# Optimization experiments

Hardware: AMD Instinct MI355X
Metric: run time of the kernel (lower is better)

The kernel has to match this reference:

```python
import jax, jax.numpy as jnp
import numpy as np

H = 128
NUM_GRAPHS = 256
NUM_TASKS = 40
BN_EPS = 1e-5


def setup_inputs() -> dict:
    key = jax.random.key(0)
    ks = jax.random.split(key, 32)
    N, E, F = 50000, 600000, 9
    inp = {}
    inp["x"] = jax.random.randint(ks[0], (N, 1), 0, 2)
    inp["edge_index"] = jax.random.randint(ks[1], (2, E), 0, N)
    inp["edge_attr"] = jax.random.uniform(ks[2], (E, F), dtype=jnp.float32)
    inp["batch"] = jnp.sort(jax.random.randint(ks[3], (N,), 0, NUM_GRAPHS))
    inp["self_loop_index"] = 7
    inp["self_loop_type"] = 1
    # parameters
    s = 0.02
    inp["node_emb"] = jax.random.normal(ks[4], (2, H), jnp.float32) * s
    for l in range(2):
        o = 5 + l * 11
        inp[f"enc_w{l}"] = jax.random.normal(ks[o + 0], (F, H), jnp.float32) * s
        inp[f"enc_b{l}"] = jnp.zeros((H,), jnp.float32)
        inp[f"w1_{l}"] = jax.random.normal(ks[o + 1], (2 * H, 2 * H), jnp.float32) * s
        inp[f"b1_{l}"] = jnp.zeros((2 * H,), jnp.float32)
        inp[f"gamma{l}"] = jnp.ones((2 * H,), jnp.float32)
        inp[f"beta{l}"] = jnp.zeros((2 * H,), jnp.float32)
        inp[f"mean{l}"] = jax.random.normal(ks[o + 2], (2 * H,), jnp.float32) * 0.1
        inp[f"var{l}"] = jax.random.uniform(ks[o + 3], (2 * H,), jnp.float32, 0.5, 1.5)
        inp[f"w2_{l}"] = jax.random.normal(ks[o + 4], (2 * H, H), jnp.float32) * s
        inp[f"b2_{l}"] = jnp.zeros((H,), jnp.float32)
    inp["pred_w"] = jax.random.normal(ks[30], (2 * H, NUM_TASKS), jnp.float32) * s
    inp["pred_b"] = jnp.zeros((NUM_TASKS,), jnp.float32)
    return inp


def _gin_layer(h, ei, ea, N, enc_w, enc_b, w1, b1, gamma, beta, mean, var, w2, b2):
    # edge encode: Linear(F, H) on all (real + self-loop) edges
    e = ea @ enc_w + enc_b                                  # [E+N, H]
    msg = jnp.concatenate([h[ei[1]], e], axis=1)            # [E+N, 2H] (feature_concat)
    agg = jax.ops.segment_sum(msg, ei[0], num_segments=N)   # sum pooling -> [N, 2H]
    z = agg @ w1 + b1
    z = (z - mean) * jax.lax.rsqrt(var + BN_EPS) * gamma + beta  # BatchNorm1d (eval)
    z = jax.nn.relu(z)
    return z @ w2 + b2                                      # [N, H]


def reference(x, edge_index, edge_attr, batch, self_loop_index, self_loop_type,
              node_emb,
              enc_w0, enc_b0, w1_0, b1_0, gamma0, beta0, mean0, var0, w2_0, b2_0,
              enc_w1, enc_b1, w1_1, b1_1, gamma1, beta1, mean1, var1, w2_1, b2_1,
              pred_w, pred_b):
    N = x.shape[0]
    loop = jnp.arange(N, dtype=edge_index.dtype)
    ei = jnp.concatenate([edge_index, jnp.stack([loop, loop])], axis=1)  # add self loops
    sl_attr = jnp.zeros((N, edge_attr.shape[1]), edge_attr.dtype).at[:, self_loop_index].set(
        jnp.asarray(self_loop_type, edge_attr.dtype))
    ea = jnp.concatenate([edge_attr, sl_attr], axis=0)       # [E+N, F]

    h0 = node_emb[x.reshape(-1)]                             # input node embedding [N, H]
    h1 = jax.nn.relu(_gin_layer(h0, ei, ea, N, enc_w0, enc_b0, w1_0, b1_0,
                                gamma0, beta0, mean0, var0, w2_0, b2_0))
    h2 = _gin_layer(h1, ei, ea, N, enc_w1, enc_b1, w1_1, b1_1,
                    gamma1, beta1, mean1, var1, w2_1, b2_1)  # JK='last'

    # graph mean pooling over batch ids
    sums = jax.ops.segment_sum(h2, batch, num_segments=NUM_GRAPHS)
    cnt = jax.ops.segment_sum(jnp.ones((N,), h2.dtype), batch, num_segments=NUM_GRAPHS)
    pooled = sums / jnp.maximum(cnt, 1.0)[:, None]
    graph_rep = jnp.concatenate([pooled, pooled], axis=1)    # no center_node_idx
    return graph_rep @ pred_w + pred_b                       # [G, num_tasks]
```

## Files before the change

kernel.cpp:

```cpp
#include <hip/hip_runtime.h>

#define H   128
#define H2  256
#define NG  256
#define NT  40
#define NF  9

typedef __attribute__((ext_vector_type(8))) short short8;
typedef __attribute__((ext_vector_type(4))) float f32x4;

#define MFMA16(a, b, c) __builtin_amdgcn_mfma_f32_16x16x32_bf16(a, b, c, 0, 0, 0)

__device__ __forceinline__ void f2bf_hilo(float x, unsigned short& hi, unsigned short& lo) {
  unsigned u = __float_as_uint(x);
  unsigned hh = (u + 0x7FFFu + ((u >> 16) & 1u)) >> 16;
  float hf = __uint_as_float(hh << 16);
  float r = x - hf;
  unsigned v = __float_as_uint(r);
  unsigned ll = (v + 0x7FFFu + ((v >> 16) & 1u)) >> 16;
  hi = (unsigned short)hh;
  lo = (unsigned short)ll;
}

__device__ __forceinline__ void cvt8(float4 a, float4 b, short8& hi, short8& lo) {
  float xs[8] = {a.x, a.y, a.z, a.w, b.x, b.y, b.z, b.w};
#pragma unroll
  for (int j = 0; j < 8; j++) {
    unsigned short h, l;
    f2bf_hilo(xs[j], h, l);
    hi[j] = (short)h;
    lo[j] = (short)l;
  }
}

__global__ void k_degc(const int* __restrict__ ei, const int* __restrict__ x,
                       unsigned* __restrict__ degc, int E) {
  int e = blockIdx.x * blockDim.x + threadIdx.x;
  if (e >= E) return;
  int dst = ei[e], src = ei[E + e];
  atomicAdd(&degc[dst], 1u + ((unsigned)x[src] << 16));
}

__global__ __launch_bounds__(1024) void k_scan(const unsigned* __restrict__ degc,
                                               unsigned* __restrict__ off,
                                               unsigned* __restrict__ cur, int N) {
  __shared__ unsigned wsum[16];
  __shared__ unsigned wpre[16];
  __shared__ unsigned s_run;
  int tid = threadIdx.x;
  int lane = tid & 63, wv = tid >> 6;
  if (tid == 0) s_run = 0u;
  __syncthreads();
  for (int base = 0; base < N; base += 4096) {
    int i0 = base + tid * 4;
    unsigned v0 = 0, v1 = 0, v2 = 0, v3 = 0;
    if (i0 + 0 < N) v0 = degc[i0 + 0] & 0xFFFFu;
    if (i0 + 1 < N) v1 = degc[i0 + 1] & 0xFFFFu;
    if (i0 + 2 < N) v2 = degc[i0 + 2] & 0xFFFFu;
    if (i0 + 3 < N) v3 = degc[i0 + 3] & 0xFFFFu;
    unsigned tsum = v0 + v1 + v2 + v3;
    unsigned sc = tsum;
#pragma unroll
    for (int d = 1; d < 64; d <<= 1) {
      unsigned t = __shfl_up(sc, d);
      if (lane >= d) sc += t;
    }
    if (lane == 63) wsum[wv] = sc;
    __syncthreads();
    if (wv == 0 && lane < 16) {
      unsigned xv = wsum[lane];
#pragma unroll
      for (int d = 1; d < 16; d <<= 1) {
        unsigned t = __shfl_up(xv, d);
        if (lane >= d) xv += t;
      }
      wpre[lane] = xv;
    }
    __syncthreads();
    unsigned excl = s_run + (wv ? wpre[wv - 1] : 0u) + (sc - tsum);
    unsigned p1 = excl + v0, p2 = p1 + v1, p3 = p2 + v2;
    if (i0 + 0 < N) { off[i0 + 0] = excl; cur[i0 + 0] = excl; }
    if (i0 + 1 < N) { off[i0 + 1] = p1;   cur[i0 + 1] = p1; }
    if (i0 + 2 < N) { off[i0 + 2] = p2;   cur[i0 + 2] = p2; }
    if (i0 + 3 < N) { off[i0 + 3] = p3;   cur[i0 + 3] = p3; }
    __syncthreads();
    if (tid == 0) s_run += wpre[15];
  }
  if (tid == 0) off[N] = s_run;
}

__global__ void k_scatter(const int* __restrict__ ei, unsigned* __restrict__ cur,
                          int* __restrict__ csrc, int* __restrict__ ceid, int E) {
  int e = blockIdx.x * blockDim.x + threadIdx.x;
  if (e >= E) return;
  int dst = ei[e], src = ei[E + e];
  unsigned pos = atomicAdd(&cur[dst], 1u);
  csrc[pos] = src;
  ceid[pos] = e;
}

__global__ __launch_bounds__(256) void k_S(const float* __restrict__ ea,
    const unsigned* __restrict__ off, const int* __restrict__ ceid,
    float* __restrict__ S, int N) {
  int lane = threadIdx.x & 63;
  int wv = threadIdx.x >> 6;
  int sub = lane & 7;
  int v = blockIdx.x * 32 + wv * 8 + (lane >> 3);
  if (v >= N) return;
  unsigned o = off[v], e = off[v + 1];
  float acc[NF];
#pragma unroll
  for (int f = 0; f < NF; f++) acc[f] = 0.f;
  for (unsigned i = o + sub; i < e; i += 8) {
    const float* a = ea + (size_t)ceid[i] * NF;
#pragma unroll
    for (int f = 0; f < NF; f++) acc[f] += a[f];
  }
#pragma unroll
  for (int d = 1; d < 8; d <<= 1)
#pragma unroll
    for (int f = 0; f < NF; f++) acc[f] += __shfl_xor(acc[f], d);
  if (sub == 0) {
#pragma unroll
    for (int f = 0; f < NF; f++) S[(size_t)v * NF + f] = acc[f];
  }
}

__global__ __launch_bounds__(256) void k_gather(const float* __restrict__ h,
    const unsigned* __restrict__ off, const int* __restrict__ csrc,
    float* __restrict__ hs, int N) {
  int v = blockIdx.x * 4 + (threadIdx.x >> 6);
  int lane = threadIdx.x & 63;
  if (v >= N) return;
  unsigned o = off[v], e = off[v + 1];
  const float2* hp = (const float2*)h;
  float2 acc = hp[(size_t)v * 64 + lane];
  float2 a0 = {0.f, 0.f}, a1 = {0.f, 0.f}, a2 = {0.f, 0.f}, a3 = {0.f, 0.f};
  unsigned i = o;
  for (; i + 4 <= e; i += 4) {
    int s0 = csrc[i], s1 = csrc[i + 1], s2 = csrc[i + 2], s3 = csrc[i + 3];
    float2 t0 = hp[(size_t)s0 * 64 + lane];
    float2 t1 = hp[(size_t)s1 * 64 + lane];
    float2 t2 = hp[(size_t)s2 * 64 + lane];
    float2 t3 = hp[(size_t)s3 * 64 + lane];
    a0.x += t0.x; a0.y += t0.y;
    a1.x += t1.x; a1.y += t1.y;
    a2.x += t2.x; a2.y += t2.y;
    a3.x += t3.x; a3.y += t3.y;
  }
  for (; i < e; i++) {
    float2 t = hp[(size_t)csrc[i] * 64 + lane];
    acc.x += t.x; acc.y += t.y;
  }
  acc.x += (a0.x + a1.x) + (a2.x + a3.x);
  acc.y += (a0.y + a1.y) + (a2.y + a3.y);
  ((float2*)hs)[(size_t)v * 64 + lane] = acc;
}

__global__ void k_prepA0(const float* __restrict__ emb,
                         const float* __restrict__ enc_w, const float* __restrict__ enc_b,
                         const float* __restrict__ w1, const float* __restrict__ b1,
                         const float* __restrict__ gamma, const float* __restrict__ beta,
                         const float* __restrict__ mean, const float* __restrict__ var,
                         const int* __restrict__ sli, const int* __restrict__ slt,
                         unsigned short* __restrict__ BAhi, unsigned short* __restrict__ BAlo,
                         float* __restrict__ cc) {
  int c = threadIdx.x;
  float e0 = 0.f, e1 = 0.f, u = 0.f;
  float m[NF];
#pragma unroll
  for (int f = 0; f < NF; f++) m[f] = 0.f;
  for (int k = 0; k < H; k++) {
    float wt = w1[(size_t)k * H2 + c];
    e0 += emb[k] * wt;
    e1 += emb[H + k] * wt;
    float wb = w1[(size_t)(H + k) * H2 + c];
#pragma unroll
    for (int f = 0; f < NF; f++) m[f] += enc_w[f * H + k] * wb;
    u += enc_b[k] * wb;
  }
  float k0 = (float)(*slt) * m[*sli] + u + b1[c];
  float scv = gamma[c] * rsqrtf(var[c] + 1e-5f);
  cc[c] = scv;
  cc[H2 + c] = beta[c] - mean[c] * scv;
  int ct = c >> 4, cl = c & 15;
  for (int k = 0; k < 32; k++) {
    float val;
    if (k == 0)       val = e0;
    else if (k == 1)  val = e1;
    else if (k < 11)  val = m[k - 2];
    else if (k == 11) val = u;
    else if (k == 12) val = k0;
    else              val = 0.f;
    unsigned short h, l;
    f2bf_hilo(val, h, l);
    int lane = (k >> 3) * 16 + cl, j = k & 7;
    size_t idx = ((size_t)(ct * 64 + lane)) * 8 + j;
    BAhi[idx] = h;
    BAlo[idx] = l;
  }
}

__global__ void k_prepA1(const float* __restrict__ enc_w, const float* __restrict__ enc_b,
                         const float* __restrict__ w1, const float* __restrict__ b1,
                         const float* __restrict__ gamma, const float* __restrict__ beta,
                         const float* __restrict__ mean, const float* __restrict__ var,
                         const int* __restrict__ sli, const int* __restrict__ slt,
                         unsigned short* __restrict__ BAhi, unsigned short* __restrict__ BAlo,
                         float* __restrict__ cc) {
  int c = threadIdx.x;
  float m[NF];
  float u = 0.f;
#pragma unroll
  for (int f = 0; f < NF; f++) m[f] = 0.f;
  for (int k = 0; k < H; k++) {
    float wv = w1[(size_t)(H + k) * H2 + c];
#pragma unroll
    for (int f = 0; f < NF; f++) m[f] += enc_w[f * H + k] * wv;
    u += enc_b[k] * wv;
  }
  float k0 = (float)(*slt) * m[*sli] + u + b1[c];
  float scv = gamma[c] * rsqrtf(var[c] + 1e-5f);
  cc[c] = scv;
  cc[H2 + c] = beta[c] - mean[c] * scv;
  int ct = c >> 4, cl = c & 15;
  for (int k = 0; k < 160; k++) {
    float val;
    if (k < 128)      val = w1[(size_t)k * H2 + c];
    else if (k < 137) val = m[k - 128];
    else if (k == 137) val = u;
    else if (k == 138) val = k0;
    else              val = 0.f;
    unsigned short h, l;
    f2bf_hilo(val, h, l);
    int ks = k >> 5, kr = k & 31;
    int lane = (kr >> 3) * 16 + cl, j = kr & 7;
    size_t idx = ((size_t)((ks * 16 + ct) * 64 + lane)) * 8 + j;
    BAhi[idx] = h;
    BAlo[idx] = l;
  }
}

__global__ void k_prepB2(const float* __restrict__ w2,
                         unsigned short* __restrict__ BBhi, unsigned short* __restrict__ BBlo) {
  int t = threadIdx.x;
  int c = t & 127, half = t >> 7;
  int ct = c >> 4, cl = c & 15;
  for (int kk = 0; kk < 128; kk++) {
    int k = half * 128 + kk;
    float val = w2[(size_t)k * H + c];
    unsigned short h, l;
    f2bf_hilo(val, h, l);
    int ks = k >> 5, kr = k & 31;
    int lane = (kr >> 3) * 16 + cl, j = kr & 7;
    size_t idx = ((size_t)((ks * 8 + ct) * 64 + lane)) * 8 + j;
    BBhi[idx] = h;
    BBlo[idx] = l;
  }
}

__global__ __launch_bounds__(256) void k_layer(
    const float* __restrict__ hs, const float* __restrict__ S,
    const unsigned* __restrict__ degc, const int* __restrict__ x,
    const unsigned short* __restrict__ BAhi, const unsigned short* __restrict__ BAlo,
    const unsigned short* __restrict__ BBhi, const unsigned short* __restrict__ BBlo,
    const float* __restrict__ cc, const float* __restrict__ b2,
    float* __restrict__ out, const int* __restrict__ batch,
    int N, int relu_out, int pool, int nks) {
  __shared__ float ext[32][36];
  __shared__ unsigned short zhi[32 * 256];
  __shared__ unsigned short zlo[32 * 256];
  int tid = threadIdx.x;
  int row0 = blockIdx.x * 32;

  for (int i = tid; i < 32 * 36; i += 256) {
    int r = i / 36, c2 = i - r * 36;
    int v = row0 + r;
    float val = 0.f;
    if (v < N) {
      unsigned pk = degc[v];
      float dg = (float)(pk & 0xFFFFu);
      float c1 = (float)(pk >> 16);
      if (nks == 0) {
        if (c2 == 0)       val = (dg - c1) + ((x[v] == 0) ? 1.f : 0.f);
        else if (c2 == 1)  val = c1 + ((x[v] != 0) ? 1.f : 0.f);
        else if (c2 < 11)  val = S[(size_t)v * NF + (c2 - 2)];
        else if (c2 == 11) val = dg;
        else if (c2 == 12) val = 1.0f;
      } else {
        if (c2 < NF)       val = S[(size_t)v * NF + c2];
        else if (c2 == 9)  val = dg;
        else if (c2 == 10) val = 1.0f;
      }
    }
    ext[r][c2] = val;
  }
  __syncthreads();

  int l = tid & 63, wv = tid >> 6;
  int rowoff = (wv >> 1) * 16;
  int ctoffA = (wv & 1) * 8;
  int lr = l & 15, lg = l >> 4;

  f32x4 acc[8];
#pragma unroll
  for (int ct = 0; ct < 8; ct++) acc[ct] = f32x4{0.f, 0.f, 0.f, 0.f};

  if (nks) {
#pragma unroll
    for (int ks = 0; ks < 4; ks++) {
      int row = row0 + rowoff + lr;
      int rowc = row < N ? row : N - 1;
      const float* src = hs + (size_t)rowc * H + ks * 32 + lg * 8;
      float4 x0 = ((const float4*)src)[0];
      float4 x1 = ((const float4*)src)[1];
      short8 ahi, alo;
      cvt8(x0, x1, ahi, alo);
#pragma unroll
      for (int ct = 0; ct < 8; ct++) {
        int gct = ctoffA + ct;
        short8 bhi = ((const short8*)BAhi)[((ks * 16 + gct) << 6) + l];
        short8 blo = ((const short8*)BAlo)[((ks * 16 + gct) << 6) + l];
        acc[ct] = MFMA16(ahi, bhi, acc[ct]);
        acc[ct] = MFMA16(ahi, blo, acc[ct]);
        acc[ct] = MFMA16(alo, bhi, acc[ct]);
      }
    }
  }
  {
    const float* src = &ext[rowoff + lr][lg * 8];
    float4 x0 = ((const float4*)src)[0];
    float4 x1 = ((const float4*)src)[1];
    short8 ahi, alo;
    cvt8(x0, x1, ahi, alo);
#pragma unroll
    for (int ct = 0; ct < 8; ct++) {
      int gct = ctoffA + ct;
      short8 bhi = ((const short8*)BAhi)[((nks * 16 + gct) << 6) + l];
      short8 blo = ((const short8*)BAlo)[((nks * 16 + gct) << 6) + l];
      acc[ct] = MFMA16(ahi, bhi, acc[ct]);
      acc[ct] = MFMA16(ahi, blo, acc[ct]);
      acc[ct] = MFMA16(alo, bhi, acc[ct]);
    }
  }

#pragma unroll
  for (int ct = 0; ct < 8; ct++) {
    int c = (ctoffA + ct) * 16 + lr;
    float scv = cc[c], shv = cc[H2 + c];
#pragma unroll
    for (int r = 0; r < 4; r++) {
      float z = acc[ct][r] * scv + shv;
      z = fmaxf(z, 0.f);
      unsigned short h, lo2;
      f2bf_hilo(z, h, lo2);
      int zr = rowoff + lg * 4 + r;
      unsigned off = (unsigned)(zr * 512 + c * 2) ^ (unsigned)((zr & 7) << 4);
      *(unsigned short*)((char*)zhi + off) = h;
      *(unsigned short*)((char*)zlo + off) = lo2;
    }
  }
  __syncthreads();

  f32x4 acc2[4];
#pragma unroll
  for (int ct = 0; ct < 4; ct++) acc2[ct] = f32x4{0.f, 0.f, 0.f, 0.f};
#pragma unroll
  for (int ks = 0; ks < 8; ks++) {
    int zr = rowoff + lr;
    unsigned off = (unsigned)(zr * 512 + (ks * 32 + lg * 8) * 2) ^ (unsigned)((zr & 7) << 4);
    short8 ahi = *(const short8*)((char*)zhi + off);
    short8 alo = *(const short8*)((char*)zlo + off);
#pragma unroll
    for (int ct = 0; ct < 4; ct++) {
      int gct = (wv & 1) * 4 + ct;
      short8 bhi = ((const short8*)BBhi)[((ks * 8 + gct) << 6) + l];
      short8 blo = ((const short8*)BBlo)[((ks * 8 + gct) << 6) + l];
      acc2[ct] = MFMA16(ahi, bhi, acc2[ct]);
      acc2[ct] = MFMA16(ahi, blo, acc2[ct]);
      acc2[ct] = MFMA16(alo, bhi, acc2[ct]);
    }
  }

#pragma unroll
  for (int ct = 0; ct < 4; ct++) {
    int c2 = ((wv & 1) * 4 + ct) * 16 + lr;
    float bias = b2[c2];
#pragma unroll
    for (int r = 0; r < 4; r++) {
      int row = row0 + rowoff + lg * 4 + r;
      if (row >= N) continue;
      float val = acc2[ct][r] + bias;
      if (relu_out) val = fmaxf(val, 0.f);
      if (pool) {
        atomicAdd(&out[(size_t)batch[row] * H + c2], val);
      } else {
        out[(size_t)row * H + c2] = val;
      }
    }
  }
}

__global__ void k_cnt(const int* __restrict__ batch, float* __restrict__ cnt, int N) {
  int v = blockIdx.x * blockDim.x + threadIdx.x;
  if (v < N) atomicAdd(&cnt[batch[v]], 1.0f);
}

__global__ void k_pred(const float* __restrict__ pooled, const float* __restrict__ cnt,
                       const float* __restrict__ pw, const float* __restrict__ pb,
                       float* __restrict__ outp) {
  int g = blockIdx.x;
  int t = threadIdx.x;
  if (t >= NT) return;
  float acc = 0.f;
  for (int k = 0; k < H; k++)
    acc += pooled[(size_t)g * H + k] * (pw[k * NT + t] + pw[(H + k) * NT + t]);
  float c = fmaxf(cnt[g], 1.0f);
  outp[(size_t)g * NT + t] = acc / c + pb[t];
}

extern "C" void kernel_launch(void* const* d_in, const int* in_sizes, int n_in,
                              void* d_out, int out_size, void* d_ws, size_t ws_size,
                              hipStream_t stream) {
  const int*   x     = (const int*)d_in[0];
  const int*   ei    = (const int*)d_in[1];
  const float* ea    = (const float*)d_in[2];
  const int*   batch = (const int*)d_in[3];
  const int*   sli   = (const int*)d_in[4];
  const int*   slt   = (const int*)d_in[5];
  const float* emb   = (const float*)d_in[6];
  const float* encw[2] = {(const float*)d_in[7],  (const float*)d_in[17]};
  const float* encb[2] = {(const float*)d_in[8],  (const float*)d_in[18]};
  const float* w1[2]   = {(const float*)d_in[9],  (const float*)d_in[19]};
  const float* b1[2]   = {(const float*)d_in[10], (const float*)d_in[20]};
  const float* gam[2]  = {(const float*)d_in[11], (const float*)d_in[21]};
  const float* bet[2]  = {(const float*)d_in[12], (const float*)d_in[22]};
  const float* mea[2]  = {(const float*)d_in[13], (const float*)d_in[23]};
  const float* var[2]  = {(const float*)d_in[14], (const float*)d_in[24]};
  const float* w2[2]   = {(const float*)d_in[15], (const float*)d_in[25]};
  const float* b2[2]   = {(const float*)d_in[16], (const float*)d_in[26]};
  const float* pw = (const float*)d_in[27];
  const float* pb = (const float*)d_in[28];

  int N = in_sizes[0];
  int E = in_sizes[1] / 2;

  char* p = (char*)d_ws;
  auto alloc = [&](size_t bytes) {
    char* r = p;
    p += (bytes + 255) / 256 * 256;
    return r;
  };
  unsigned* degc   = (unsigned*)alloc((size_t)N * 4);
  float*    S      = (float*)alloc((size_t)N * NF * 4);
  unsigned* off    = (unsigned*)alloc((size_t)(N + 1) * 4);
  unsigned* cur    = (unsigned*)alloc((size_t)N * 4);
  int*      csrc   = (int*)alloc((size_t)E * 4);
  int*      ceid   = (int*)alloc((size_t)E * 4);
  float*    hB     = (float*)alloc((size_t)N * H * 4);
  float*    hS     = (float*)alloc((size_t)N * H * 4);
  unsigned short* BA0hi = (unsigned short*)alloc((size_t)16 * 64 * 8 * 2);
  unsigned short* BA0lo = (unsigned short*)alloc((size_t)16 * 64 * 8 * 2);
  unsigned short* BA1hi = (unsigned short*)alloc((size_t)5 * 16 * 64 * 8 * 2);
  unsigned short* BA1lo = (unsigned short*)alloc((size_t)5 * 16 * 64 * 8 * 2);
  unsigned short* BB0hi = (unsigned short*)alloc((size_t)8 * 8 * 64 * 8 * 2);
  unsigned short* BB0lo = (unsigned short*)alloc((size_t)8 * 8 * 64 * 8 * 2);
  unsigned short* BB1hi = (unsigned short*)alloc((size_t)8 * 8 * 64 * 8 * 2);
  unsigned short* BB1lo = (unsigned short*)alloc((size_t)8 * 8 * 64 * 8 * 2);
  float*    cc0    = (float*)alloc((size_t)2 * H2 * 4);
  float*    cc1    = (float*)alloc((size_t)2 * H2 * 4);
  float*    pooled = (float*)alloc((size_t)NG * H * 4);
  float*    cnt    = (float*)alloc((size_t)NG * 4);

  hipMemsetAsync(degc, 0, (size_t)N * 4, stream);
  hipMemsetAsync(pooled, 0, (size_t)NG * H * 4, stream);
  hipMemsetAsync(cnt, 0, (size_t)NG * 4, stream);

  int nblk = (N + 31) / 32;

  k_degc<<<(E + 255) / 256, 256, 0, stream>>>(ei, x, degc, E);
  k_scan<<<1, 1024, 0, stream>>>(degc, off, cur, N);
  k_scatter<<<(E + 255) / 256, 256, 0, stream>>>(ei, cur, csrc, ceid, E);
  k_S<<<(N + 31) / 32, 256, 0, stream>>>(ea, off, ceid, S, N);

  k_prepA0<<<1, 256, 0, stream>>>(emb, encw[0], encb[0], w1[0], b1[0], gam[0], bet[0],
                                  mea[0], var[0], sli, slt, BA0hi, BA0lo, cc0);
  k_prepB2<<<1, 256, 0, stream>>>(w2[0], BB0hi, BB0lo);
  k_prepA1<<<1, 256, 0, stream>>>(encw[1], encb[1], w1[1], b1[1], gam[1], bet[1],
                                  mea[1], var[1], sli, slt, BA1hi, BA1lo, cc1);
  k_prepB2<<<1, 256, 0, stream>>>(w2[1], BB1hi, BB1lo);

  k_layer<<<nblk, 256, 0, stream>>>(nullptr, S, degc, x, BA0hi, BA0lo, BB0hi, BB0lo,
                                    cc0, b2[0], hB, batch, N, 1, 0, 0);
  k_gather<<<(N + 3) / 4, 256, 0, stream>>>(hB, off, csrc, hS, N);
  k_layer<<<nblk, 256, 0, stream>>>(hS, S, degc, x, BA1hi, BA1lo, BB1hi, BB1lo,
                                    cc1, b2[1], pooled, batch, N, 0, 1, 4);

  k_cnt<<<(N + 255) / 256, 256, 0, stream>>>(batch, cnt, N);
  k_pred<<<NG, 64, 0, stream>>>(pooled, cnt, pw, pb, (float*)d_out);
}
```

Measured before the change: 679.9 us.

## Retile layer GEMM to 64 rows, emit bf16 hi/lo from gather, vectorize loads

The fused layer kernel now handles 64 rows per block. Each wave reuses its B fragments across four row fragments in the first GEMM and across two in the second, which cuts repeated global weight loads. The gather kernel unrolls to eight independent neighbor loads and writes its sums as split bf16 hi/lo arrays, so the layer kernel reads ready-made MFMA operands instead of converting fp32. The edge-attribute sum loads use wider vector reads. In exchange, shared memory per block doubles, the grid has fewer blocks, and register pressure rises, which can lower occupancy.

```diff
diff --git a/kernel.cpp b/kernel.cpp
--- a/kernel.cpp
+++ b/kernel.cpp
@@ -8,6 +8,8 @@
 
 typedef __attribute__((ext_vector_type(8))) short short8;
 typedef __attribute__((ext_vector_type(4))) float f32x4;
+typedef float float4u __attribute__((ext_vector_type(4)));
+typedef float4u float4ua __attribute__((aligned(4)));
 
 #define MFMA16(a, b, c) __builtin_amdgcn_mfma_f32_16x16x32_bf16(a, b, c, 0, 0, 0)
 
@@ -113,8 +115,12 @@
   for (int f = 0; f < NF; f++) acc[f] = 0.f;
   for (unsigned i = o + sub; i < e; i += 8) {
     const float* a = ea + (size_t)ceid[i] * NF;
-#pragma unroll
-    for (int f = 0; f < NF; f++) acc[f] += a[f];
+    float4u v0 = ((const float4ua*)a)[0];
+    float4u v1 = ((const float4ua*)a)[1];
+    float v8 = a[8];
+    acc[0] += v0.x; acc[1] += v0.y; acc[2] += v0.z; acc[3] += v0.w;
+    acc[4] += v1.x; acc[5] += v1.y; acc[6] += v1.z; acc[7] += v1.w;
+    acc[8] += v8;
   }
 #pragma unroll
   for (int d = 1; d < 8; d <<= 1)
@@ -128,33 +134,38 @@
 
 __global__ __launch_bounds__(256) void k_gather(const float* __restrict__ h,
     const unsigned* __restrict__ off, const int* __restrict__ csrc,
-    float* __restrict__ hs, int N) {
+    unsigned short* __restrict__ hsHi, unsigned short* __restrict__ hsLo, int N) {
   int v = blockIdx.x * 4 + (threadIdx.x >> 6);
   int lane = threadIdx.x & 63;
   if (v >= N) return;
   unsigned o = off[v], e = off[v + 1];
   const float2* hp = (const float2*)h;
   float2 acc = hp[(size_t)v * 64 + lane];
-  float2 a0 = {0.f, 0.f}, a1 = {0.f, 0.f}, a2 = {0.f, 0.f}, a3 = {0.f, 0.f};
+  float2 a[8];
+#pragma unroll
+  for (int j = 0; j < 8; j++) a[j] = make_float2(0.f, 0.f);
   unsigned i = o;
-  for (; i + 4 <= e; i += 4) {
-    int s0 = csrc[i], s1 = csrc[i + 1], s2 = csrc[i + 2], s3 = csrc[i + 3];
-    float2 t0 = hp[(size_t)s0 * 64 + lane];
-    float2 t1 = hp[(size_t)s1 * 64 + lane];
-    float2 t2 = hp[(size_t)s2 * 64 + lane];
-    float2 t3 = hp[(size_t)s3 * 64 + lane];
-    a0.x += t0.x; a0.y += t0.y;
-    a1.x += t1.x; a1.y += t1.y;
-    a2.x += t2.x; a2.y += t2.y;
-    a3.x += t3.x; a3.y += t3.y;
+  for (; i + 8 <= e; i += 8) {
+    int s[8];
+#pragma unroll
+    for (int j = 0; j < 8; j++) s[j] = csrc[i + j];
+#pragma unroll
+    for (int j = 0; j < 8; j++) {
+      float2 t = hp[(size_t)s[j] * 64 + lane];
+      a[j].x += t.x; a[j].y += t.y;
+    }
   }
   for (; i < e; i++) {
     float2 t = hp[(size_t)csrc[i] * 64 + lane];
     acc.x += t.x; acc.y += t.y;
   }
-  acc.x += (a0.x + a1.x) + (a2.x + a3.x);
-  acc.y += (a0.y + a1.y) + (a2.y + a3.y);
-  ((float2*)hs)[(size_t)v * 64 + lane] = acc;
+#pragma unroll
+  for (int j = 0; j < 8; j++) { acc.x += a[j].x; acc.y += a[j].y; }
+  unsigned short h0, l0, h1, l1;
+  f2bf_hilo(acc.x, h0, l0);
+  f2bf_hilo(acc.y, h1, l1);
+  ((unsigned*)hsHi)[(size_t)v * 64 + lane] = (unsigned)h0 | ((unsigned)h1 << 16);
+  ((unsigned*)hsLo)[(size_t)v * 64 + lane] = (unsigned)l0 | ((unsigned)l1 << 16);
 }
 
 __global__ void k_prepA0(const float* __restrict__ emb,
@@ -260,21 +271,22 @@
 }
 
 __global__ __launch_bounds__(256) void k_layer(
-    const float* __restrict__ hs, const float* __restrict__ S,
-    const unsigned* __restrict__ degc, const int* __restrict__ x,
+    const unsigned short* __restrict__ hsHi, const unsigned short* __restrict__ hsLo,
+    const float* __restrict__ S, const unsigned* __restrict__ degc,
+    const int* __restrict__ x,
     const unsigned short* __restrict__ BAhi, const unsigned short* __restrict__ BAlo,
     const unsigned short* __restrict__ BBhi, const unsigned short* __restrict__ BBlo,
     const float* __restrict__ cc, const float* __restrict__ b2,
     float* __restrict__ out, const int* __restrict__ batch,
     int N, int relu_out, int pool, int nks) {
-  __shared__ float ext[32][36];
-  __shared__ unsigned short zhi[32 * 256];
-  __shared__ unsigned short zlo[32 * 256];
+  __shared__ float ext[64][36];
+  __shared__ unsigned short zhi[64 * 256];
+  __shared__ unsigned short zlo[64 * 256];
   int tid = threadIdx.x;
-  int row0 = blockIdx.x * 32;
-
-  for (int i = tid; i < 32 * 36; i += 256) {
-    int r = i / 36, c2 = i - r * 36;
+  int row0 = blockIdx.x * 64;
+
+  for (int i = tid; i < 64 * 32; i += 256) {
+    int r = i >> 5, c2 = i & 31;
     int v = row0 + r;
     float val = 0.f;
     if (v < N) {
@@ -298,104 +310,141 @@
   __syncthreads();
 
   int l = tid & 63, wv = tid >> 6;
-  int rowoff = (wv >> 1) * 16;
-  int ctoffA = (wv & 1) * 8;
   int lr = l & 15, lg = l >> 4;
 
-  f32x4 acc[8];
-#pragma unroll
-  for (int ct = 0; ct < 8; ct++) acc[ct] = f32x4{0.f, 0.f, 0.f, 0.f};
+  f32x4 acc[4][4];
+#pragma unroll
+  for (int rf = 0; rf < 4; rf++)
+#pragma unroll
+    for (int ct = 0; ct < 4; ct++) acc[rf][ct] = f32x4{0.f, 0.f, 0.f, 0.f};
 
   if (nks) {
 #pragma unroll
     for (int ks = 0; ks < 4; ks++) {
-      int row = row0 + rowoff + lr;
-      int rowc = row < N ? row : N - 1;
-      const float* src = hs + (size_t)rowc * H + ks * 32 + lg * 8;
+      short8 ah[4], al[4];
+#pragma unroll
+      for (int rf = 0; rf < 4; rf++) {
+        int row = row0 + rf * 16 + lr;
+        int rowc = row < N ? row : N - 1;
+        ah[rf] = *(const short8*)(hsHi + (size_t)rowc * H + ks * 32 + lg * 8);
+        al[rf] = *(const short8*)(hsLo + (size_t)rowc * H + ks * 32 + lg * 8);
+      }
+      short8 bh[4], bl[4];
+#pragma unroll
+      for (int ct = 0; ct < 4; ct++) {
+        int gct = wv * 4 + ct;
+        bh[ct] = ((const short8*)BAhi)[((ks * 16 + gct) << 6) + l];
+        bl[ct] = ((const short8*)BAlo)[((ks * 16 + gct) << 6) + l];
+      }
+#pragma unroll
+      for (int ct = 0; ct < 4; ct++)
+#pragma unroll
+        for (int rf = 0; rf < 4; rf++) {
+          acc[rf][ct] = MFMA16(ah[rf], bh[ct], acc[rf][ct]);
+          acc[rf][ct] = MFMA16(ah[rf], bl[ct], acc[rf][ct]);
+          acc[rf][ct] = MFMA16(al[rf], bh[ct], acc[rf][ct]);
+        }
+    }
+  }
+  {
+    short8 ah[4], al[4];
+#pragma unroll
+    for (int rf = 0; rf < 4; rf++) {
+      const float* src = &ext[rf * 16 + lr][lg * 8];
       float4 x0 = ((const float4*)src)[0];
       float4 x1 = ((const float4*)src)[1];
-      short8 ahi, alo;
-      cvt8(x0, x1, ahi, alo);
-#pragma unroll
-      for (int ct = 0; ct < 8; ct++) {
-        int gct = ctoffA + ct;
-        short8 bhi = ((const short8*)BAhi)[((ks * 16 + gct) << 6) + l];
-        short8 blo = ((const short8*)BAlo)[((ks * 16 + gct) << 6) + l];
-        acc[ct] = MFMA16(ahi, bhi, acc[ct]);
-        acc[ct] = MFMA16(ahi, blo, acc[ct]);
-        acc[ct] = MFMA16(alo, bhi, acc[ct]);
-      }
-    }
-  }
-  {
-    const float* src = &ext[rowoff + lr][lg * 8];
-    float4 x0 = ((const float4*)src)[0];
-    float4 x1 = ((const float4*)src)[1];
-    short8 ahi, alo;
-    cvt8(x0, x1, ahi, alo);
-#pragma unroll
-    for (int ct = 0; ct < 8; ct++) {
-      int gct = ctoffA + ct;
-      short8 bhi = ((const short8*)BAhi)[((nks * 16 + gct) << 6) + l];
-      short8 blo = ((const short8*)BAlo)[((nks * 16 + gct) << 6) + l];
-      acc[ct] = MFMA16(ahi, bhi, acc[ct]);
-      acc[ct] = MFMA16(ahi, blo, acc[ct]);
-      acc[ct] = MFMA16(alo, bhi, acc[ct]);
-    }
-  }
-
-#pragma unroll
-  for (int ct = 0; ct < 8; ct++) {
-    int c = (ctoffA + ct) * 16 + lr;
+      cvt8(x0, x1, ah[rf], al[rf]);
+    }
+    short8 bh[4], bl[4];
+#pragma unroll
+    for (int ct = 0; ct < 4; ct++) {
+      int gct = wv * 4 + ct;
+      bh[ct] = ((const short8*)BAhi)[((nks * 16 + gct) << 6) + l];
+      bl[ct] = ((const short8*)BAlo)[((nks * 16 + gct) << 6) + l];
+    }
+#pragma unroll
+    for (int ct = 0; ct < 4; ct++)
+#pragma unroll
+      for (int rf = 0; rf < 4; rf++) {
+        acc[rf][ct] = MFMA16(ah[rf], bh[ct], acc[rf][ct]);
+        acc[rf][ct] = MFMA16(ah[rf], bl[ct], acc[rf][ct]);
+        acc[rf][ct] = MFMA16(al[rf], bh[ct], acc[rf][ct]);
+      }
+  }
+
+#pragma unroll
+  for (int ct = 0; ct < 4; ct++) {
+    int c = (wv * 4 + ct) * 16 + lr;
     float scv = cc[c], shv = cc[H2 + c];
 #pragma unroll
-    for (int r = 0; r < 4; r++) {
-      float z = acc[ct][r] * scv + shv;
-      z = fmaxf(z, 0.f);
-      unsigned short h, lo2;
-      f2bf_hilo(z, h, lo2);
-      int zr = rowoff + lg * 4 + r;
-      unsigned off = (unsigned)(zr * 512 + c * 2) ^ (unsigned)((zr & 7) << 4);
-      *(unsigned short*)((char*)zhi + off) = h;
-      *(unsigned short*)((char*)zlo + off) = lo2;
+    for (int rf = 0; rf < 4; rf++) {
+#pragma unroll
+      for (int r = 0; r < 4; r++) {
+        float z = acc[rf][ct][r] * scv + shv;
+        z = fmaxf(z, 0.f);
+        unsigned short h, lo2;
+        f2bf_hilo(z, h, lo2);
+        int zr = rf * 16 + lg * 4 + r;
+        unsigned off = (unsigned)(zr * 512 + c * 2) ^ (unsigned)((zr & 7) << 4);
+        *(unsigned short*)((char*)zhi + off) = h;
+        *(unsigned short*)((char*)zlo + off) = lo2;
+      }
     }
   }
   __syncthreads();
 
-  f32x4 acc2[4];
-#pragma unroll
-  for (int ct = 0; ct < 4; ct++) acc2[ct] = f32x4{0.f, 0.f, 0.f, 0.f};
+  int r0b = (wv >> 1) * 32;
+  int cb = wv & 1;
+  f32x4 acc2[2][4];
+#pragma unroll
+  for (int rf = 0; rf < 2; rf++)
+#pragma unroll
+    for (int ct = 0; ct < 4; ct++) acc2[rf][ct] = f32x4{0.f, 0.f, 0.f, 0.f};
+
 #pragma unroll
   for (int ks = 0; ks < 8; ks++) {
-    int zr = rowoff + lr;
-    unsigned off = (unsigned)(zr * 512 + (ks * 32 + lg * 8) * 2) ^ (unsigned)((zr & 7) << 4);
-    short8 ahi = *(const short8*)((char*)zhi + off);
-    short8 alo = *(const short8*)((char*)zlo + off);
+    short8 zah[2], zal[2];
+#pragma unroll
+    for (int rf = 0; rf < 2; rf++) {
+      int zr = r0b + rf * 16 + lr;
+      unsigned off = (unsigned)(zr * 512 + (ks * 32 + lg * 8) * 2) ^ (unsigned)((zr & 7) << 4);
+      zah[rf] = *(const short8*)((char*)zhi + off);
+      zal[rf] = *(const short8*)((char*)zlo + off);
+    }
+    short8 bh[4], bl[4];
 #pragma unroll
     for (int ct = 0; ct < 4; ct++) {
-      int gct = (wv & 1) * 4 + ct;
-      short8 bhi = ((const short8*)BBhi)[((ks * 8 + gct) << 6) + l];
-      short8 blo = ((const short8*)BBlo)[((ks * 8 + gct) << 6) + l];
-      acc2[ct] = MFMA16(ahi, bhi, acc2[ct]);
-      acc2[ct] = MFMA16(ahi, blo, acc2[ct]);
-      acc2[ct] = MFMA16(alo, bhi, acc2[ct]);
-    }
+      int gct = cb * 4 + ct;
+      bh[ct] = ((const short8*)BBhi)[((ks * 8 + gct) << 6) + l];
+      bl[ct] = ((const short8*)BBlo)[((ks * 8 + gct) << 6) + l];
+    }
+#pragma unroll
+    for (int ct = 0; ct < 4; ct++)
+#pragma unroll
+      for (int rf = 0; rf < 2; rf++) {
+        acc2[rf][ct] = MFMA16(zah[rf], bh[ct], acc2[rf][ct]);
+        acc2[rf][ct] = MFMA16(zah[rf], bl[ct], acc2[rf][ct]);
+        acc2[rf][ct] = MFMA16(zal[rf], bh[ct], acc2[rf][ct]);
+      }
   }
 
 #pragma unroll
   for (int ct = 0; ct < 4; ct++) {
-    int c2 = ((wv & 1) * 4 + ct) * 16 + lr;
+    int c2 = (cb * 4 + ct) * 16 + lr;
     float bias = b2[c2];
 #pragma unroll
-    for (int r = 0; r < 4; r++) {
-      int row = row0 + rowoff + lg * 4 + r;
-      if (row >= N) continue;
-      float val = acc2[ct][r] + bias;
-      if (relu_out) val = fmaxf(val, 0.f);
-      if (pool) {
-        atomicAdd(&out[(size_t)batch[row] * H + c2], val);
-      } else {
-        out[(size_t)row * H + c2] = val;
+    for (int rf = 0; rf < 2; rf++) {
+#pragma unroll
+      for (int r = 0; r < 4; r++) {
+        int row = row0 + r0b + rf * 16 + lg * 4 + r;
+        if (row >= N) continue;
+        float val = acc2[rf][ct][r] + bias;
+        if (relu_out) val = fmaxf(val, 0.f);
+        if (pool) {
+          atomicAdd(&out[(size_t)batch[row] * H + c2], val);
+        } else {
+          out[(size_t)row * H + c2] = val;
+        }
       }
     }
   }
@@ -458,7 +507,8 @@
   int*      csrc   = (int*)alloc((size_t)E * 4);
   int*      ceid   = (int*)alloc((size_t)E * 4);
   float*    hB     = (float*)alloc((size_t)N * H * 4);
-  float*    hS     = (float*)alloc((size_t)N * H * 4);
+  unsigned short* hsHi = (unsigned short*)alloc((size_t)N * H * 2);
+  unsigned short* hsLo = (unsigned short*)alloc((size_t)N * H * 2);
   unsigned short* BA0hi = (unsigned short*)alloc((size_t)16 * 64 * 8 * 2);
   unsigned short* BA0lo = (unsigned short*)alloc((size_t)16 * 64 * 8 * 2);
   unsigned short* BA1hi = (unsigned short*)alloc((size_t)5 * 16 * 64 * 8 * 2);
@@ -476,7 +526,7 @@
   hipMemsetAsync(pooled, 0, (size_t)NG * H * 4, stream);
   hipMemsetAsync(cnt, 0, (size_t)NG * 4, stream);
 
-  int nblk = (N + 31) / 32;
+  int nblk = (N + 63) / 64;
 
   k_degc<<<(E + 255) / 256, 256, 0, stream>>>(ei, x, degc, E);
   k_scan<<<1, 1024, 0, stream>>>(degc, off, cur, N);
@@ -490,10 +540,12 @@
                                   mea[1], var[1], sli, slt, BA1hi, BA1lo, cc1);
   k_prepB2<<<1, 256, 0, stream>>>(w2[1], BB1hi, BB1lo);
 
-  k_layer<<<nblk, 256, 0, stream>>>(nullptr, S, degc, x, BA0hi, BA0lo, BB0hi, BB0lo,
+  k_layer<<<nblk, 256, 0, stream>>>(nullptr, nullptr, S, degc, x,
+                                    BA0hi, BA0lo, BB0hi, BB0lo,
                                     cc0, b2[0], hB, batch, N, 1, 0, 0);
-  k_gather<<<(N + 3) / 4, 256, 0, stream>>>(hB, off, csrc, hS, N);
-  k_layer<<<nblk, 256, 0, stream>>>(hS, S, degc, x, BA1hi, BA1lo, BB1hi, BB1lo,
+  k_gather<<<(N + 3) / 4, 256, 0, stream>>>(hB, off, csrc, hsHi, hsLo, N);
+  k_layer<<<nblk, 256, 0, stream>>>(hsHi, hsLo, S, degc, x,
+                                    BA1hi, BA1lo, BB1hi, BB1lo,
                                     cc1, b2[1], pooled, batch, N, 0, 1, 4);
 
   k_cnt<<<(N + 255) / 256, 256, 0, stream>>>(batch, cnt, N);
```

Measured after the change: 696.4 us. 2.4% more time.
